# Performance work log

Measured on AMD Instinct MI355X. Metric: run time of the kernel, lower is better.

## Reference

```python
import jax, jax.numpy as jnp
import numpy as np

WS = 7   # window_size
SS = 3   # shift_size = window_size // 2
NH = 16  # num_heads


def _rel_pos_index(ws):
    coords = np.stack(np.meshgrid(np.arange(ws), np.arange(ws), indexing='ij'))  # (2, ws, ws)
    cf = coords.reshape(2, -1)
    rel = (cf[:, :, None] - cf[:, None, :]).transpose(1, 2, 0)
    rel[:, :, 0] += ws - 1
    rel[:, :, 1] += ws - 1
    rel[:, :, 0] *= 2 * ws - 1
    return rel.sum(-1)  # (ws*ws, ws*ws) int

REL_IDX = _rel_pos_index(WS)


def _attn_mask(h, w, ws, ss):
    img = np.zeros((h, w))
    sls = (slice(0, -ws), slice(-ws, -ss), slice(-ss, None))
    cnt = 0
    for i in sls:
        for j in sls:
            img[i, j] = cnt
            cnt += 1
    mw = img.reshape(h // ws, ws, w // ws, ws).transpose(0, 2, 1, 3).reshape(-1, ws * ws)
    d = mw[:, None, :] - mw[:, :, None]  # (nW, N, N)
    return np.where(d != 0, -100.0, 0.0).astype(np.float32)


def _part(x, ws):
    b, h, w, c = x.shape
    return x.reshape(b, h // ws, ws, w // ws, ws, c).transpose(0, 1, 3, 2, 4, 5).reshape(-1, ws * ws, c)


def _rev(win, ws, h, w):
    c = win.shape[-1]
    b = win.shape[0] // ((h // ws) * (w // ws))
    return win.reshape(b, h // ws, w // ws, ws, ws, c).transpose(0, 1, 3, 2, 4, 5).reshape(b, h, w, c)


def _ln(x, g, b):
    m = x.mean(-1, keepdims=True)
    v = x.var(-1, keepdims=True)
    return (x - m) / jnp.sqrt(v + 1e-5) * g + b


def _wattn(x, qkv_w, qkv_b, proj_w, proj_b, table, mask):
    B_, N, C = x.shape
    hd = C // NH
    scale = hd ** -0.5
    qkv = (x @ qkv_w.T + qkv_b).reshape(B_, N, 3, NH, hd).transpose(2, 0, 3, 1, 4)
    q, k, v = qkv[0] * scale, qkv[1], qkv[2]  # (B_, NH, N, hd)
    attn = jnp.einsum('bhnd,bhmd->bhnm', q, k)
    bias = table[REL_IDX.reshape(-1)].reshape(N, N, NH).transpose(2, 0, 1)  # (NH, N, N)
    attn = attn + bias[None]
    if mask is not None:
        nW = mask.shape[0]
        attn = (attn.reshape(B_ // nW, nW, NH, N, N) + mask[None, :, None]).reshape(B_, NH, N, N)
    attn = jax.nn.softmax(attn, axis=-1)
    out = jnp.einsum('bhnm,bhmd->bhnd', attn, v).transpose(0, 2, 1, 3).reshape(B_, N, C)
    return out @ proj_w.T + proj_b


def _mlp(x, w1, b1, w2, b2):
    return jax.nn.gelu(x @ w1.T + b1, approximate=False) @ w2.T + b2


def _forward(x, w_norm1_g, w_norm1_b, w_qkv_w, w_qkv_b, w_proj_w, w_proj_b, w_table,
             w_norm2_g, w_norm2_b, w_fc1_w, w_fc1_b, w_fc2_w, w_fc2_b,
             sw_norm1_g, sw_norm1_b, sw_qkv_w, sw_qkv_b, sw_proj_w, sw_proj_b, sw_table,
             sw_norm2_g, sw_norm2_b, sw_fc1_w, sw_fc1_b, sw_fc2_w, sw_fc2_b):
    b, c, h, w = x.shape
    x = jnp.transpose(x, (0, 2, 3, 1)).reshape(b, h * w, c)  # (B, HW, C)
    shortcut = x
    xn = _ln(x, w_norm1_g, w_norm1_b).reshape(b, h, w, c)
    aw = _wattn(_part(xn, WS), w_qkv_w, w_qkv_b, w_proj_w, w_proj_b, w_table, None)
    x = shortcut + _rev(aw, WS, h, w).reshape(b, h * w, c)
    x = x + _mlp(_ln(x, w_norm2_g, w_norm2_b), w_fc1_w, w_fc1_b, w_fc2_w, w_fc2_b)
    # shifted-window branch (shift_size > 0 since min(h,w) > window_size)
    xn = _ln(x, sw_norm1_g, sw_norm1_b)
    mask = jnp.asarray(_attn_mask(h, w, WS, SS))
    shifted = jnp.roll(xn.reshape(b, h, w, c), (-SS, -SS), axis=(1, 2))
    sa = _wattn(_part(shifted, WS), sw_qkv_w, sw_qkv_b, sw_proj_w, sw_proj_b, sw_table, mask)
    shifted = jnp.roll(_rev(sa, WS, h, w), (SS, SS), axis=(1, 2)).reshape(b, h * w, c)
    # NOTE: source adds the residual to the *normalized* activations here; kept faithful.
    x = xn + shifted
    x = x + _mlp(_ln(x, sw_norm2_g, sw_norm2_b), sw_fc1_w, sw_fc1_b, sw_fc2_w, sw_fc2_b)
    return x.reshape(b, h, w, c)


def setup_inputs() -> dict:
    key = jax.random.key(0)
    ks = jax.random.split(key, 32)
    B, C, H, W = 8, 512, 56, 56
    Cm = 4 * C
    T = (2 * WS - 1) ** 2

    def rn(k, shape, s=0.02):
        return jax.random.normal(k, shape, jnp.float32) * s

    d = {'x': jax.random.normal(ks[0], (B, C, H, W), jnp.float32)}
    for i, p in enumerate(['w', 'sw']):
        o = 1 + i * 6
        d[p + '_norm1_g'] = jnp.ones((C,), jnp.float32)
        d[p + '_norm1_b'] = jnp.zeros((C,), jnp.float32)
        d[p + '_qkv_w'] = rn(ks[o], (3 * C, C))
        d[p + '_qkv_b'] = jnp.zeros((3 * C,), jnp.float32)
        d[p + '_proj_w'] = rn(ks[o + 1], (C, C))
        d[p + '_proj_b'] = jnp.zeros((C,), jnp.float32)
        d[p + '_table'] = rn(ks[o + 2], (T, NH))
        d[p + '_norm2_g'] = jnp.ones((C,), jnp.float32)
        d[p + '_norm2_b'] = jnp.zeros((C,), jnp.float32)
        d[p + '_fc1_w'] = rn(ks[o + 3], (Cm, C))
        d[p + '_fc1_b'] = jnp.zeros((Cm,), jnp.float32)
        d[p + '_fc2_w'] = rn(ks[o + 4], (C, Cm))
        d[p + '_fc2_b'] = jnp.zeros((C,), jnp.float32)
    return d


def reference(x, w_norm1_g, w_norm1_b, w_qkv_w, w_qkv_b, w_proj_w, w_proj_b, w_table,
              w_norm2_g, w_norm2_b, w_fc1_w, w_fc1_b, w_fc2_w, w_fc2_b,
              sw_norm1_g, sw_norm1_b, sw_qkv_w, sw_qkv_b, sw_proj_w, sw_proj_b, sw_table,
              sw_norm2_g, sw_norm2_b, sw_fc1_w, sw_fc1_b, sw_fc2_w, sw_fc2_b):
    return _forward(x, w_norm1_g, w_norm1_b, w_qkv_w, w_qkv_b, w_proj_w, w_proj_b, w_table,
                    w_norm2_g, w_norm2_b, w_fc1_w, w_fc1_b, w_fc2_w, w_fc2_b,
                    sw_norm1_g, sw_norm1_b, sw_qkv_w, sw_qkv_b, sw_proj_w, sw_proj_b, sw_table,
                    sw_norm2_g, sw_norm2_b, sw_fc1_w, sw_fc1_b, sw_fc2_w, sw_fc2_b)
```

## Files before the change

### kernel.cpp

```cpp
#include <hip/hip_runtime.h>
#include <hip/hip_bf16.h>

using bf16 = __hip_bfloat16;

#define B_      8
#define C_      512
#define H_      56
#define W_      56
#define HW_     3136
#define M_      25088
#define NH_     16
#define HD_     32
#define WS_     7
#define NT_     49

typedef __attribute__((ext_vector_type(8))) short bf16x8;
typedef __attribute__((ext_vector_type(4))) float f32x4;

#define AS1(p) ((const __attribute__((address_space(1))) void*)(p))
#define AS3(p) ((__attribute__((address_space(3))) void*)(p))

__device__ inline float bf2f(const bf16 v) {
    unsigned short u = *reinterpret_cast<const unsigned short*>(&v);
    return __uint_as_float((unsigned)u << 16);
}
__device__ inline unsigned short f2bfu(float f) {
    bf16 h = __float2bfloat16(f);
    return *reinterpret_cast<unsigned short*>(&h);
}
__device__ inline float rdv(const float* p) { return *p; }
__device__ inline float rdv(const bf16* p)  { return bf2f(*p); }
__device__ inline void stv(float* p, float v) { *p = v; }
__device__ inline void stv(bf16* p, float v)  { *p = __float2bfloat16(v); }

__global__ void k_detect(const void* g1, int* flag) {
    const unsigned short* u = (const unsigned short*)g1;
    *flag = (u[0] == 0x3F80u) ? 1 : 0;
}

struct WArgs {
    const void* src[26];
    bf16*       dst[26];
    int         n[26];
};
__global__ __launch_bounds__(256) void k_convert_all(WArgs a, const int* flag) {
    const int isb = *flag;
    const int gid = blockIdx.x * 256 + threadIdx.x;
    const int stride = gridDim.x * 256;
    #pragma unroll 1
    for (int w = 0; w < 26; ++w) {
        const int n = a.n[w];
        bf16* d = a.dst[w];
        if (isb) {
            const unsigned short* s = (const unsigned short*)a.src[w];
            for (int i = gid; i < n; i += stride) ((unsigned short*)d)[i] = s[i];
        } else {
            const float* s = (const float*)a.src[w];
            for (int i = gid; i < n; i += stride) d[i] = __float2bfloat16(s[i]);
        }
    }
}

__global__ __launch_bounds__(256) void k_transpose_in(const void* xin, bf16* X,
                                                      const int* flag) {
    __shared__ float tile[32][33];
    const int isb = *flag;
    const int p0 = blockIdx.x * 32, c0 = blockIdx.y * 32, b = blockIdx.z;
    const int tp = threadIdx.x & 31, tc = threadIdx.x >> 5;
    const size_t ibase = (size_t)b * C_ * HW_;
    #pragma unroll
    for (int i = 0; i < 4; ++i) {
        const int c = tc + i * 8;
        const size_t idx = ibase + (size_t)(c0 + c) * HW_ + p0 + tp;
        tile[c][tp] = isb ? bf2f(((const bf16*)xin)[idx]) : ((const float*)xin)[idx];
    }
    __syncthreads();
    const int wc = threadIdx.x & 31, wp = threadIdx.x >> 5;
    bf16* dst = X + (size_t)b * HW_ * C_;
    #pragma unroll
    for (int i = 0; i < 4; ++i) {
        const int p = wp + i * 8;
        dst[(size_t)(p0 + p) * C_ + c0 + wc] = __float2bfloat16(tile[wc][p]);
    }
}

__global__ __launch_bounds__(128) void k_layernorm(const bf16* __restrict__ X,
                                                   const bf16* __restrict__ g,
                                                   const bf16* __restrict__ bta,
                                                   bf16* __restrict__ XN) {
    const int tok = blockIdx.x;
    const ushort4 u = reinterpret_cast<const ushort4*>(X + (size_t)tok * C_)[threadIdx.x];
    float4 v;
    v.x = __uint_as_float((unsigned)u.x << 16);
    v.y = __uint_as_float((unsigned)u.y << 16);
    v.z = __uint_as_float((unsigned)u.z << 16);
    v.w = __uint_as_float((unsigned)u.w << 16);
    float s  = v.x + v.y + v.z + v.w;
    float s2 = v.x * v.x + v.y * v.y + v.z * v.z + v.w * v.w;
    #pragma unroll
    for (int o = 32; o > 0; o >>= 1) { s += __shfl_down(s, o); s2 += __shfl_down(s2, o); }
    __shared__ float sh[4];
    if ((threadIdx.x & 63) == 0) { sh[threadIdx.x >> 6] = s; sh[2 + (threadIdx.x >> 6)] = s2; }
    __syncthreads();
    const float ts = sh[0] + sh[1], ts2 = sh[2] + sh[3];
    const float m = ts * (1.0f / C_);
    const float var = ts2 * (1.0f / C_) - m * m;
    const float r = rsqrtf(var + 1e-5f);
    const int c = threadIdx.x * 4;
    ushort4 o;
    o.x = f2bfu((v.x - m) * r * bf2f(g[c + 0]) + bf2f(bta[c + 0]));
    o.y = f2bfu((v.y - m) * r * bf2f(g[c + 1]) + bf2f(bta[c + 1]));
    o.z = f2bfu((v.z - m) * r * bf2f(g[c + 2]) + bf2f(bta[c + 2]));
    o.w = f2bfu((v.w - m) * r * bf2f(g[c + 3]) + bf2f(bta[c + 3]));
    reinterpret_cast<ushort4*>(XN + (size_t)tok * C_)[threadIdx.x] = o;
}

template <typename TADD, typename TO, bool GELU, bool ADD, bool FINAL>
__global__ __launch_bounds__(256, 2) void k_gemm_mfma(const bf16* __restrict__ A,
                                                      const bf16* __restrict__ Wt,
                                                      const bf16* __restrict__ bias,
                                                      const TADD* __restrict__ addp,
                                                      TO* __restrict__ out,
                                                      const int* flag,
                                                      int rowBase, int N, int K) {
    __shared__ bf16 sA[2][128 * 64];
    __shared__ bf16 sB[2][128 * 64];
    const int tid  = threadIdx.x;
    const int lane = tid & 63;
    const int wid  = tid >> 6;
    const int wr   = wid >> 1;
    const int wc2  = wid & 1;

    const int nwg  = gridDim.x;
    const int orig = blockIdx.x;
    const int nx = nwg >> 3, rr_ = nwg & 7;
    const int xcd = orig & 7, offw = orig >> 3;
    const int wg = (xcd < rr_ ? xcd * (nx + 1) : rr_ * (nx + 1) + (xcd - rr_) * nx) + offw;
    const int gx = N >> 7;
    const int m0 = (wg / gx) * 128, n0 = (wg % gx) * 128;

    const f32x4 vz = {0.f, 0.f, 0.f, 0.f};
    f32x4 acc[4][4];
    #pragma unroll
    for (int i = 0; i < 4; ++i)
        #pragma unroll
        for (int j = 0; j < 4; ++j) acc[i][j] = vz;

    const int sr8  = lane >> 3;
    const int schk = (lane & 7) ^ sr8;
    const bf16* gA0 = A  + (size_t)(m0 + sr8) * K + schk * 8;
    const bf16* gB0 = Wt + (size_t)(n0 + sr8) * K + schk * 8;

    const int l15 = lane & 15, g4 = lane >> 4;
    const int NTLE = K >> 6;

    int cur = 0;
    {
        #pragma unroll
        for (int p = 0; p < 4; ++p) {
            const int q = wid * 4 + p;
            __builtin_amdgcn_global_load_lds(AS1(gA0 + (size_t)(q * 8) * K),
                                             AS3(&sA[0][q * 512]), 16, 0, 0);
            __builtin_amdgcn_global_load_lds(AS1(gB0 + (size_t)(q * 8) * K),
                                             AS3(&sB[0][q * 512]), 16, 0, 0);
        }
    }

    for (int t = 0; t < NTLE; ++t) {
        asm volatile("s_waitcnt vmcnt(0)" ::: "memory");
        __builtin_amdgcn_s_barrier();

        if (t + 1 < NTLE) {
            const int kt = (t + 1) << 6;
            #pragma unroll
            for (int p = 0; p < 4; ++p) {
                const int q = wid * 4 + p;
                __builtin_amdgcn_global_load_lds(AS1(gA0 + (size_t)(q * 8) * K + kt),
                                                 AS3(&sA[cur ^ 1][q * 512]), 16, 0, 0);
                __builtin_amdgcn_global_load_lds(AS1(gB0 + (size_t)(q * 8) * K + kt),
                                                 AS3(&sB[cur ^ 1][q * 512]), 16, 0, 0);
            }
        }

        bf16x8 af[4][2], bf_[4][2];
        #pragma unroll
        for (int ks = 0; ks < 2; ++ks) {
            const int ch = ((ks << 2) | g4) ^ (l15 & 7);
            #pragma unroll
            for (int f = 0; f < 4; ++f) {
                const int rowA = wr * 64 + f * 16 + l15;
                af[f][ks] = *reinterpret_cast<const bf16x8*>(&sA[cur][rowA * 64 + ch * 8]);
                const int rowB = wc2 * 64 + f * 16 + l15;
                bf_[f][ks] = *reinterpret_cast<const bf16x8*>(&sB[cur][rowB * 64 + ch * 8]);
            }
        }

        __builtin_amdgcn_s_setprio(1);
        #pragma unroll
        for (int i = 0; i < 4; ++i)
            #pragma unroll
            for (int j = 0; j < 4; ++j) {
                acc[i][j] = __builtin_amdgcn_mfma_f32_16x16x32_bf16(af[i][0], bf_[j][0], acc[i][j], 0, 0, 0);
                acc[i][j] = __builtin_amdgcn_mfma_f32_16x16x32_bf16(af[i][1], bf_[j][1], acc[i][j], 0, 0, 0);
            }
        __builtin_amdgcn_s_setprio(0);

        asm volatile("s_waitcnt lgkmcnt(0)" ::: "memory");
        __builtin_amdgcn_s_barrier();
        cur ^= 1;
    }

    int obf = 0;
    if constexpr (FINAL) obf = *flag;
    const int colBase = n0 + wc2 * 64 + l15;
    const int rowTop  = rowBase + m0 + wr * 64 + g4 * 4;
    #pragma unroll
    for (int j = 0; j < 4; ++j) {
        const int col = colBase + j * 16;
        const float bc = bf2f(bias[col]);
        #pragma unroll
        for (int i = 0; i < 4; ++i) {
            #pragma unroll
            for (int r = 0; r < 4; ++r) {
                const int row = rowTop + i * 16 + r;
                float v = acc[i][j][r] + bc;
                if constexpr (GELU) v = 0.5f * v * (1.0f + erff(v * 0.70710678118654752f));
                if constexpr (ADD)  v += rdv(&addp[(size_t)row * N + col]);
                if constexpr (FINAL) {
                    if (obf) ((bf16*)(void*)out)[(size_t)row * N + col] = __float2bfloat16(v);
                    else     ((float*)(void*)out)[(size_t)row * N + col] = v;
                } else {
                    stv(&out[(size_t)row * N + col], v);
                }
            }
        }
    }
}

__global__ __launch_bounds__(256) void k_mktbl(const bf16* __restrict__ table,
                                               bf16* __restrict__ out, int shifted) {
    const int bh = blockIdx.x;
    const int cls = bh >> 4, h = bh & 15;
    const int rowE = shifted ? (cls >> 1) : 0;
    const int colE = shifted ? (cls & 1) : 0;
    for (int e = threadIdx.x; e < 64 * 64; e += 256) {
        const int i = e >> 6, j = e & 63;
        float v;
        if (i < NT_ && j < NT_) {
            const int yi = i / WS_, xi = i % WS_, yj = j / WS_, xj = j % WS_;
            const int ridx = (yi - yj + 6) * 13 + (xi - xj + 6);
            v = bf2f(table[ridx * NH_ + h]);
            const int ri = (rowE ? (yi < 4 ? 1 : 2) : 0) * 3 + (colE ? (xi < 4 ? 1 : 2) : 0);
            const int rj = (rowE ? (yj < 4 ? 1 : 2) : 0) * 3 + (colE ? (xj < 4 ? 1 : 2) : 0);
            if (ri != rj) v -= 100.f;
        } else if (j >= NT_) {
            v = -3e30f;
        } else {
            v = 0.f;
        }
        out[((size_t)bh << 12) + e] = __float2bfloat16(v);
    }
}

template <int SS, bool SHIFTED>
__global__ __launch_bounds__(64) void k_attn_mfma(const bf16* __restrict__ QKV,
                                                  const bf16* __restrict__ tbl,
                                                  bf16* __restrict__ O) {
    __shared__ __align__(16) short uQK[5120];
    __shared__ __align__(16) short uVt[2304];
    __shared__ int toks[NT_];
    short* Qs = uQK;
    short* Ks = uQK + 2560;
    short* Ps = uQK;

    const int lane = threadIdx.x;
    const int head = blockIdx.x & 15;
    const int win  = blockIdx.x >> 4;
    const int bl = win >> 6, w64 = win & 63;
    const int wy = w64 >> 3, wx = w64 & 7;

    if (lane < NT_) {
        const int dy = lane / WS_, dx = lane % WS_;
        const int sr = wy * WS_ + dy, scn = wx * WS_ + dx;
        const int r = (sr + SS) % H_, c = (scn + SS) % W_;
        toks[lane] = bl * HW_ + r * W_ + c;
    }
    __syncthreads();

    const int g4 = lane >> 4, l15 = lane & 15;
    const int tsg = lane >> 2, csg = (lane & 3) * 8;

    #pragma unroll
    for (int rr = 0; rr < 4; ++rr) {
        const int t = rr * 16 + tsg;
        bf16x8 qv = {0,0,0,0,0,0,0,0}, kv = {0,0,0,0,0,0,0,0}, vv = {0,0,0,0,0,0,0,0};
        if (t < NT_) {
            const bf16* base = QKV + (size_t)toks[t] * 1536 + head * HD_ + csg;
            qv = *reinterpret_cast<const bf16x8*>(base);
            kv = *reinterpret_cast<const bf16x8*>(base + 512);
            vv = *reinterpret_cast<const bf16x8*>(base + 1024);
        }
        *reinterpret_cast<bf16x8*>(&Qs[t * 40 + csg]) = qv;
        *reinterpret_cast<bf16x8*>(&Ks[t * 40 + csg]) = kv;
        #pragma unroll
        for (int e = 0; e < 8; ++e) uVt[(csg + e) * 72 + t] = ((const short*)&vv)[e];
    }
    __syncthreads();

    bf16x8 aq[4], bk[4];
    #pragma unroll
    for (int f = 0; f < 4; ++f) {
        aq[f] = *reinterpret_cast<const bf16x8*>(&Qs[(f * 16 + l15) * 40 + g4 * 8]);
        bk[f] = *reinterpret_cast<const bf16x8*>(&Ks[(f * 16 + l15) * 40 + g4 * 8]);
    }
    const f32x4 vz = {0.f, 0.f, 0.f, 0.f};
    f32x4 sacc[4][4];
    #pragma unroll
    for (int qi = 0; qi < 4; ++qi)
        #pragma unroll
        for (int kj = 0; kj < 4; ++kj)
            sacc[qi][kj] = __builtin_amdgcn_mfma_f32_16x16x32_bf16(aq[qi], bk[kj], vz, 0, 0, 0);
    __syncthreads();

    const int cls = SHIFTED ? (((wy == 7) ? 2 : 0) + ((wx == 7) ? 1 : 0)) : 0;
    const bf16* tb = tbl + (((size_t)(cls * NH_ + head)) << 12);
    const float scale = 0.17677669529663687f;
    #pragma unroll
    for (int qi = 0; qi < 4; ++qi) {
        #pragma unroll
        for (int r = 0; r < 4; ++r) {
            const int i = qi * 16 + g4 * 4 + r;
            const bf16* trow = tb + (i << 6);
            float sv[4];
            #pragma unroll
            for (int kj = 0; kj < 4; ++kj)
                sv[kj] = sacc[qi][kj][r] * scale + bf2f(trow[kj * 16 + l15]);
            float mx = fmaxf(fmaxf(sv[0], sv[1]), fmaxf(sv[2], sv[3]));
            #pragma unroll
            for (int d = 1; d <= 8; d <<= 1) mx = fmaxf(mx, __shfl_xor(mx, d));
            float p[4], sum = 0.f;
            #pragma unroll
            for (int kj = 0; kj < 4; ++kj) { p[kj] = __expf(sv[kj] - mx); sum += p[kj]; }
            #pragma unroll
            for (int d = 1; d <= 8; d <<= 1) sum += __shfl_xor(sum, d);
            const float inv = 1.0f / sum;
            #pragma unroll
            for (int kj = 0; kj < 4; ++kj)
                Ps[i * 72 + kj * 16 + l15] = (short)f2bfu(p[kj] * inv);
        }
    }
    __syncthreads();

    f32x4 oacc[4][2];
    #pragma unroll
    for (int qi = 0; qi < 4; ++qi) { oacc[qi][0] = vz; oacc[qi][1] = vz; }
    #pragma unroll
    for (int ks = 0; ks < 2; ++ks) {
        bf16x8 bv[2];
        #pragma unroll
        for (int dj = 0; dj < 2; ++dj)
            bv[dj] = *reinterpret_cast<const bf16x8*>(&uVt[(dj * 16 + l15) * 72 + ks * 32 + g4 * 8]);
        #pragma unroll
        for (int qi = 0; qi < 4; ++qi) {
            const bf16x8 ap = *reinterpret_cast<const bf16x8*>(&Ps[(qi * 16 + l15) * 72 + ks * 32 + g4 * 8]);
            #pragma unroll
            for (int dj = 0; dj < 2; ++dj)
                oacc[qi][dj] = __builtin_amdgcn_mfma_f32_16x16x32_bf16(ap, bv[dj], oacc[qi][dj], 0, 0, 0);
        }
    }
    #pragma unroll
    for (int qi = 0; qi < 4; ++qi) {
        #pragma unroll
        for (int r = 0; r < 4; ++r) {
            const int i = qi * 16 + g4 * 4 + r;
            if (i < NT_) {
                const size_t ob = (size_t)toks[i] * C_ + head * HD_ + l15;
                O[ob]      = __float2bfloat16(oacc[qi][0][r]);
                O[ob + 16] = __float2bfloat16(oacc[qi][1][r]);
            }
        }
    }
}

extern "C" void kernel_launch(void* const* d_in, const int* in_sizes, int n_in,
                              void* d_out, int out_size, void* d_ws, size_t ws_size,
                              hipStream_t stream) {
    (void)out_size;
    char* ws = (char*)d_ws;
    const size_t WEIGHT_RESERVE = 12651520;
    bf16*  WC   = (bf16*)ws;
    int*   FLG  = (int*)(ws + WEIGHT_RESERVE);
    bf16*  TBL1 = (bf16*)(ws + WEIGHT_RESERVE + 1024);
    bf16*  TBL2 = (bf16*)(ws + WEIGHT_RESERVE + 1024 + 131072);
    bf16*  X    = (bf16*)(ws + WEIGHT_RESERVE + 656384);
    bf16*  XN   = X + (size_t)M_ * C_;
    char*  BIG  = (char*)(XN + (size_t)M_ * C_);

    const size_t full_need = WEIGHT_RESERVE + 656384 + (size_t)M_ * C_ * 4 + (size_t)M_ * 2048 * 2;
    const int IMGS = (ws_size >= full_need) ? B_ : 2;
    const int NCHUNK = B_ / IMGS;
    const int ROWS = IMGS * HW_;

    size_t offs[27];
    size_t off = 0;
    for (int i = 1; i < n_in && i < 27; ++i) { offs[i] = off; off += (size_t)((in_sizes[i] + 7) & ~7); }
    auto wc = [&](int i) { return (const bf16*)(WC + offs[i]); };

    k_detect<<<1, 1, 0, stream>>>(d_in[1], FLG);
    {
        WArgs a;
        for (int i = 1; i < 27; ++i) {
            a.src[i - 1] = d_in[i];
            a.dst[i - 1] = WC + offs[i];
            a.n[i - 1]   = in_sizes[i];
        }
        k_convert_all<<<512, 256, 0, stream>>>(a, FLG);
    }
    k_mktbl<<<16, 256, 0, stream>>>(wc(7),  TBL1, 0);
    k_mktbl<<<64, 256, 0, stream>>>(wc(20), TBL2, 1);

    const dim3 gT(HW_ / 32, C_ / 32, B_);
    k_transpose_in<<<gT, 256, 0, stream>>>(d_in[0], X, FLG);

    bf16* QKV = (bf16*)BIG;
    bf16* ATT = (bf16*)(BIG + (size_t)ROWS * 1536 * 2);
    bf16* HID = (bf16*)BIG;

    const int gQ = (1536 / 128) * (ROWS / 128);
    const int gP = (512 / 128)  * (ROWS / 128);
    const int gF = (2048 / 128) * (ROWS / 128);
    const dim3 gA(IMGS * 64 * NH_);

    k_layernorm<<<M_, 128, 0, stream>>>(X, wc(1), wc(2), XN);
    for (int c = 0; c < NCHUNK; ++c) {
        const size_t ro = (size_t)c * ROWS;
        k_gemm_mfma<bf16, bf16, false, false, false><<<gQ, 256, 0, stream>>>(
            XN + ro * C_, wc(3), wc(4), (const bf16*)nullptr, QKV, nullptr, 0, 1536, C_);
        k_attn_mfma<0, false><<<gA, 64, 0, stream>>>(QKV, TBL1, ATT);
        k_gemm_mfma<bf16, bf16, false, true, false><<<gP, 256, 0, stream>>>(
            ATT, wc(5), wc(6), X, X, nullptr, (int)ro, C_, C_);
    }
    k_layernorm<<<M_, 128, 0, stream>>>(X, wc(8), wc(9), XN);
    for (int c = 0; c < NCHUNK; ++c) {
        const size_t ro = (size_t)c * ROWS;
        k_gemm_mfma<bf16, bf16, true, false, false><<<gF, 256, 0, stream>>>(
            XN + ro * C_, wc(10), wc(11), (const bf16*)nullptr, HID, nullptr, 0, 2048, C_);
        k_gemm_mfma<bf16, bf16, false, true, false><<<gP, 256, 0, stream>>>(
            HID, wc(12), wc(13), X, X, nullptr, (int)ro, C_, 2048);
    }
    k_layernorm<<<M_, 128, 0, stream>>>(X, wc(14), wc(15), XN);
    for (int c = 0; c < NCHUNK; ++c) {
        const size_t ro = (size_t)c * ROWS;
        k_gemm_mfma<bf16, bf16, false, false, false><<<gQ, 256, 0, stream>>>(
            XN + ro * C_, wc(16), wc(17), (const bf16*)nullptr, QKV, nullptr, 0, 1536, C_);
        k_attn_mfma<3, true><<<gA, 64, 0, stream>>>(QKV, TBL2, ATT);
        k_gemm_mfma<bf16, bf16, false, true, false><<<gP, 256, 0, stream>>>(
            ATT, wc(18), wc(19), XN, X, nullptr, (int)ro, C_, C_);
    }
    k_layernorm<<<M_, 128, 0, stream>>>(X, wc(21), wc(22), XN);
    for (int c = 0; c < NCHUNK; ++c) {
        const size_t ro = (size_t)c * ROWS;
        k_gemm_mfma<bf16, bf16, true, false, false><<<gF, 256, 0, stream>>>(
            XN + ro * C_, wc(23), wc(24), (const bf16*)nullptr, HID, nullptr, 0, 2048, C_);
        k_gemm_mfma<bf16, float, false, true, true><<<gP, 256, 0, stream>>>(
            HID, wc(25), wc(26), X, (float*)d_out, FLG, (int)ro, C_, 2048);
    }
}
```

Baseline: 796.5 us.

## Enlarge GEMM tiles to 256x256, drop image chunking, use tanh GELU

```diff
diff --git a/kernel.cpp b/kernel.cpp
--- a/kernel.cpp
+++ b/kernel.cpp
@@ -32,6 +32,12 @@
 __device__ inline float rdv(const bf16* p)  { return bf2f(*p); }
 __device__ inline void stv(float* p, float v) { *p = v; }
 __device__ inline void stv(bf16* p, float v)  { *p = __float2bfloat16(v); }
+
+__device__ inline float gelu_t(float v) {
+    const float u = v * (0.79788456080286536f + 0.035677408136300125f * v * v);
+    const float e = __expf(2.0f * u);
+    return 0.5f * v * (2.0f - 2.0f / (e + 1.0f));
+}
 
 __global__ void k_detect(const void* g1, int* flag) {
     const unsigned short* u = (const unsigned short*)g1;
@@ -116,33 +122,33 @@
 }
 
 template <typename TADD, typename TO, bool GELU, bool ADD, bool FINAL>
-__global__ __launch_bounds__(256, 2) void k_gemm_mfma(const bf16* __restrict__ A,
+__global__ __launch_bounds__(512, 2) void k_gemm_mfma(const bf16* __restrict__ A,
                                                       const bf16* __restrict__ Wt,
                                                       const bf16* __restrict__ bias,
                                                       const TADD* __restrict__ addp,
                                                       TO* __restrict__ out,
                                                       const int* flag,
-                                                      int rowBase, int N, int K) {
-    __shared__ bf16 sA[2][128 * 64];
-    __shared__ bf16 sB[2][128 * 64];
+                                                      int N, int K) {
+    __shared__ bf16 sA[2][256 * 64];
+    __shared__ bf16 sB[2][256 * 64];
     const int tid  = threadIdx.x;
     const int lane = tid & 63;
     const int wid  = tid >> 6;
-    const int wr   = wid >> 1;
-    const int wc2  = wid & 1;
+    const int wr   = wid >> 2;
+    const int wc2  = wid & 3;
 
     const int nwg  = gridDim.x;
     const int orig = blockIdx.x;
     const int nx = nwg >> 3, rr_ = nwg & 7;
     const int xcd = orig & 7, offw = orig >> 3;
     const int wg = (xcd < rr_ ? xcd * (nx + 1) : rr_ * (nx + 1) + (xcd - rr_) * nx) + offw;
-    const int gx = N >> 7;
-    const int m0 = (wg / gx) * 128, n0 = (wg % gx) * 128;
+    const int gx = N >> 8;
+    const int m0 = (wg / gx) * 256, n0 = (wg % gx) * 256;
 
     const f32x4 vz = {0.f, 0.f, 0.f, 0.f};
-    f32x4 acc[4][4];
-    #pragma unroll
-    for (int i = 0; i < 4; ++i)
+    f32x4 acc[8][4];
+    #pragma unroll
+    for (int i = 0; i < 8; ++i)
         #pragma unroll
         for (int j = 0; j < 4; ++j) acc[i][j] = vz;
 
@@ -182,27 +188,30 @@
             }
         }
 
-        bf16x8 af[4][2], bf_[4][2];
+        bf16x8 bfr[4][2];
         #pragma unroll
         for (int ks = 0; ks < 2; ++ks) {
             const int ch = ((ks << 2) | g4) ^ (l15 & 7);
             #pragma unroll
-            for (int f = 0; f < 4; ++f) {
-                const int rowA = wr * 64 + f * 16 + l15;
-                af[f][ks] = *reinterpret_cast<const bf16x8*>(&sA[cur][rowA * 64 + ch * 8]);
-                const int rowB = wc2 * 64 + f * 16 + l15;
-                bf_[f][ks] = *reinterpret_cast<const bf16x8*>(&sB[cur][rowB * 64 + ch * 8]);
+            for (int j = 0; j < 4; ++j) {
+                const int rowB = wc2 * 64 + j * 16 + l15;
+                bfr[j][ks] = *reinterpret_cast<const bf16x8*>(&sB[cur][rowB * 64 + ch * 8]);
             }
         }
-
+        const int ch0 = g4 ^ (l15 & 7);
+        const int ch1 = (4 | g4) ^ (l15 & 7);
         __builtin_amdgcn_s_setprio(1);
         #pragma unroll
-        for (int i = 0; i < 4; ++i)
+        for (int i = 0; i < 8; ++i) {
+            const int rowA = wr * 128 + i * 16 + l15;
+            const bf16x8 a0 = *reinterpret_cast<const bf16x8*>(&sA[cur][rowA * 64 + ch0 * 8]);
+            const bf16x8 a1 = *reinterpret_cast<const bf16x8*>(&sA[cur][rowA * 64 + ch1 * 8]);
             #pragma unroll
             for (int j = 0; j < 4; ++j) {
-                acc[i][j] = __builtin_amdgcn_mfma_f32_16x16x32_bf16(af[i][0], bf_[j][0], acc[i][j], 0, 0, 0);
-                acc[i][j] = __builtin_amdgcn_mfma_f32_16x16x32_bf16(af[i][1], bf_[j][1], acc[i][j], 0, 0, 0);
+                acc[i][j] = __builtin_amdgcn_mfma_f32_16x16x32_bf16(a0, bfr[j][0], acc[i][j], 0, 0, 0);
+                acc[i][j] = __builtin_amdgcn_mfma_f32_16x16x32_bf16(a1, bfr[j][1], acc[i][j], 0, 0, 0);
             }
+        }
         __builtin_amdgcn_s_setprio(0);
 
         asm volatile("s_waitcnt lgkmcnt(0)" ::: "memory");
@@ -213,18 +222,18 @@
     int obf = 0;
     if constexpr (FINAL) obf = *flag;
     const int colBase = n0 + wc2 * 64 + l15;
-    const int rowTop  = rowBase + m0 + wr * 64 + g4 * 4;
+    const int rowTop  = m0 + wr * 128 + g4 * 4;
     #pragma unroll
     for (int j = 0; j < 4; ++j) {
         const int col = colBase + j * 16;
         const float bc = bf2f(bias[col]);
         #pragma unroll
-        for (int i = 0; i < 4; ++i) {
+        for (int i = 0; i < 8; ++i) {
             #pragma unroll
             for (int r = 0; r < 4; ++r) {
                 const int row = rowTop + i * 16 + r;
                 float v = acc[i][j][r] + bc;
-                if constexpr (GELU) v = 0.5f * v * (1.0f + erff(v * 0.70710678118654752f));
+                if constexpr (GELU) v = gelu_t(v);
                 if constexpr (ADD)  v += rdv(&addp[(size_t)row * N + col]);
                 if constexpr (FINAL) {
                     if (obf) ((bf16*)(void*)out)[(size_t)row * N + col] = __float2bfloat16(v);
@@ -385,7 +394,7 @@
 extern "C" void kernel_launch(void* const* d_in, const int* in_sizes, int n_in,
                               void* d_out, int out_size, void* d_ws, size_t ws_size,
                               hipStream_t stream) {
-    (void)out_size;
+    (void)out_size; (void)ws_size;
     char* ws = (char*)d_ws;
     const size_t WEIGHT_RESERVE = 12651520;
     bf16*  WC   = (bf16*)ws;
@@ -396,11 +405,6 @@
     bf16*  XN   = X + (size_t)M_ * C_;
     char*  BIG  = (char*)(XN + (size_t)M_ * C_);
 
-    const size_t full_need = WEIGHT_RESERVE + 656384 + (size_t)M_ * C_ * 4 + (size_t)M_ * 2048 * 2;
-    const int IMGS = (ws_size >= full_need) ? B_ : 2;
-    const int NCHUNK = B_ / IMGS;
-    const int ROWS = IMGS * HW_;
-
     size_t offs[27];
     size_t off = 0;
     for (int i = 1; i < n_in && i < 27; ++i) { offs[i] = off; off += (size_t)((in_sizes[i] + 7) & ~7); }
@@ -423,46 +427,34 @@
     k_transpose_in<<<gT, 256, 0, stream>>>(d_in[0], X, FLG);
 
     bf16* QKV = (bf16*)BIG;
-    bf16* ATT = (bf16*)(BIG + (size_t)ROWS * 1536 * 2);
+    bf16* ATT = (bf16*)(BIG + (size_t)M_ * 1536 * 2);
     bf16* HID = (bf16*)BIG;
 
-    const int gQ = (1536 / 128) * (ROWS / 128);
-    const int gP = (512 / 128)  * (ROWS / 128);
-    const int gF = (2048 / 128) * (ROWS / 128);
-    const dim3 gA(IMGS * 64 * NH_);
+    const int gQ = (1536 / 256) * (M_ / 256);
+    const int gP = (512 / 256)  * (M_ / 256);
+    const int gF = (2048 / 256) * (M_ / 256);
+    const dim3 gA(B_ * 64 * NH_);
 
     k_layernorm<<<M_, 128, 0, stream>>>(X, wc(1), wc(2), XN);
-    for (int c = 0; c < NCHUNK; ++c) {
-        const size_t ro = (size_t)c * ROWS;
-        k_gemm_mfma<bf16, bf16, false, false, false><<<gQ, 256, 0, stream>>>(
-            XN + ro * C_, wc(3), wc(4), (const bf16*)nullptr, QKV, nullptr, 0, 1536, C_);
-        k_attn_mfma<0, false><<<gA, 64, 0, stream>>>(QKV, TBL1, ATT);
-        k_gemm_mfma<bf16, bf16, false, true, false><<<gP, 256, 0, stream>>>(
-            ATT, wc(5), wc(6), X, X, nullptr, (int)ro, C_, C_);
-    }
+    k_gemm_mfma<bf16, bf16, false, false, false><<<gQ, 512, 0, stream>>>(
+        XN, wc(3), wc(4), (const bf16*)nullptr, QKV, nullptr, 1536, C_);
+    k_attn_mfma<0, false><<<gA, 64, 0, stream>>>(QKV, TBL1, ATT);
+    k_gemm_mfma<bf16, bf16, false, true, false><<<gP, 512, 0, stream>>>(
+        ATT, wc(5), wc(6), X, X, nullptr, C_, C_);
     k_layernorm<<<M_, 128, 0, stream>>>(X, wc(8), wc(9), XN);
-    for (int c = 0; c < NCHUNK; ++c) {
-        const size_t ro = (size_t)c * ROWS;
-        k_gemm_mfma<bf16, bf16, true, false, false><<<gF, 256, 0, stream>>>(
-            XN + ro * C_, wc(10), wc(11), (const bf16*)nullptr, HID, nullptr, 0, 2048, C_);
-        k_gemm_mfma<bf16, bf16, false, true, false><<<gP, 256, 0, stream>>>(
-            HID, wc(12), wc(13), X, X, nullptr, (int)ro, C_, 2048);
-    }
+    k_gemm_mfma<bf16, bf16, true, false, false><<<gF, 512, 0, stream>>>(
+        XN, wc(10), wc(11), (const bf16*)nullptr, HID, nullptr, 2048, C_);
+    k_gemm_mfma<bf16, bf16, false, true, false><<<gP, 512, 0, stream>>>(
+        HID, wc(12), wc(13), X, X, nullptr, C_, 2048);
     k_layernorm<<<M_, 128, 0, stream>>>(X, wc(14), wc(15), XN);
-    for (int c = 0; c < NCHUNK; ++c) {
-        const size_t ro = (size_t)c * ROWS;
-        k_gemm_mfma<bf16, bf16, false, false, false><<<gQ, 256, 0, stream>>>(
-            XN + ro * C_, wc(16), wc(17), (const bf16*)nullptr, QKV, nullptr, 0, 1536, C_);
-        k_attn_mfma<3, true><<<gA, 64, 0, stream>>>(QKV, TBL2, ATT);
-        k_gemm_mfma<bf16, bf16, false, true, false><<<gP, 256, 0, stream>>>(
-            ATT, wc(18), wc(19), XN, X, nullptr, (int)ro, C_, C_);
-    }
+    k_gemm_mfma<bf16, bf16, false, false, false><<<gQ, 512, 0, stream>>>(
+        XN, wc(16), wc(17), (const bf16*)nullptr, QKV, nullptr, 1536, C_);
+    k_attn_mfma<3, true><<<gA, 64, 0, stream>>>(QKV, TBL2, ATT);
+    k_gemm_mfma<bf16, bf16, false, true, false><<<gP, 512, 0, stream>>>(
+        ATT, wc(18), wc(19), XN, X, nullptr, C_, C_);
     k_layernorm<<<M_, 128, 0, stream>>>(X, wc(21), wc(22), XN);
-    for (int c = 0; c < NCHUNK; ++c) {
-        const size_t ro = (size_t)c * ROWS;
-        k_gemm_mfma<bf16, bf16, true, false, false><<<gF, 256, 0, stream>>>(
-            XN + ro * C_, wc(23), wc(24), (const bf16*)nullptr, HID, nullptr, 0, 2048, C_);
-        k_gemm_mfma<bf16, float, false, true, true><<<gP, 256, 0, stream>>>(
-            HID, wc(25), wc(26), X, (float*)d_out, FLG, (int)ro, C_, 2048);
-    }
-}
+    k_gemm_mfma<bf16, bf16, true, false, false><<<gF, 512, 0, stream>>>(
+        XN, wc(23), wc(24), (const bf16*)nullptr, HID, nullptr, 2048, C_);
+    k_gemm_mfma<bf16, float, false, true, true><<<gP, 512, 0, stream>>>(
+        HID, wc(25), wc(26), X, (float*)d_out, FLG, C_, 2048);
+}
```

Result: slower. 910.5 us (+14.3%).
